# Kernel optimization log

Hardware: AMD Instinct MI355X
Metric: run time of the kernel (lower is better)

Reference implementation:

```python
import jax, jax.numpy as jnp
import numpy as np

N_ITEMS = 100000
EMBED_DIM = 64
N_REL = 3
N_EDGES = 3200000


def setup_inputs() -> dict:
    key = jax.random.key(0)
    k1, k2, k3, k4 = jax.random.split(key, 4)
    item_embeddings = jax.random.normal(k1, (N_ITEMS, EMBED_DIM), dtype=jnp.float32)
    rows = jax.random.randint(k2, (N_REL, N_EDGES), 0, N_ITEMS, dtype=jnp.int64)
    cols = jax.random.randint(k3, (N_REL, N_EDGES), 0, N_ITEMS, dtype=jnp.int64)
    vals = jax.random.uniform(k4, (N_REL, N_EDGES), dtype=jnp.float32)
    return {"item_embeddings": item_embeddings, "rows": rows, "cols": cols, "vals": vals}


def reference(item_embeddings, rows, cols, vals):
    # item_embeddings: [N, D]; rows/cols/vals: [R, E] COO edge lists per relation.
    n_items, _ = item_embeddings.shape
    n_rel = rows.shape[0]
    rel_emb = jnp.zeros_like(item_embeddings)
    for r in range(n_rel):  # fixed small number of relation types
        # SpMM: neighbor_emb[i] = sum_{e: rows[e]==i} vals[e] * E[cols[e]]
        msgs = item_embeddings[cols[r]] * vals[r][:, None]          # [E, D]
        neighbor = jax.ops.segment_sum(msgs, rows[r], num_segments=n_items)  # [N, D]
        # degree = row sum of adjacency values, clamped to min 1
        degree = jax.ops.segment_sum(vals[r], rows[r], num_segments=n_items)  # [N]
        degree = jnp.maximum(degree, 1.0)
        rel_emb = rel_emb + neighbor / degree[:, None]
    rel_emb = rel_emb / n_rel
    return item_embeddings + rel_emb
```

## Files before the change

### kernel.cpp

```cpp
#include <hip/hip_runtime.h>

#define N_ITEMS     100000
#define EMBED_DIM   64
#define N_REL       3
#define N_EDGES     3200000
#define TOTAL_EDGES (N_REL * N_EDGES)
#define NKEY        (N_REL * N_ITEMS)

#define LOG_CH   6
#define CH_ROWS  64
#define NCHUNK   1563
#define NBKT     (NCHUNK * N_REL)
#define BCAP     2368
#define LOG_CB   12
#define NCB      25
#define TILEP    2048
#define NTILEP   ((N_EDGES + TILEP - 1) / TILEP)
#define SEGSB    68
#define CBCAP    (SEGSB * TILEP)

__global__ void initall_kernel(unsigned* __restrict__ gcursorF,
                               unsigned* __restrict__ cursorC) {
    int i = blockIdx.x * 256 + threadIdx.x;
    if (i < NBKT) gcursorF[i] = (unsigned)i * (unsigned)BCAP;
    if (i < N_REL * NCB) cursorC[i] = (unsigned)(i % NCB) * (unsigned)CBCAP;
}

__global__ void tobf16_kernel(const float* __restrict__ E, unsigned short* __restrict__ Ebf) {
    int i = blockIdx.x * 256 + threadIdx.x;
    if (i < N_ITEMS * EMBED_DIM) {
        unsigned u = __float_as_uint(E[i]);
        unsigned r = (u + 0x7FFFu + ((u >> 16) & 1u)) >> 16;
        Ebf[i] = (unsigned short)r;
    }
}

__launch_bounds__(512)
__global__ void partA2_kernel(const int* __restrict__ rows,
                              const int* __restrict__ cols,
                              const float* __restrict__ vals,
                              unsigned* __restrict__ cursorC,
                              uint2* __restrict__ coarse,
                              int rel0, unsigned relStrideU2) {
    __shared__ uint2 stag[TILEP];
    __shared__ unsigned char bkt[TILEP];
    __shared__ unsigned hist[NCB], lstart[NCB], gbase[NCB], lcur[NCB];
    int rel = rel0 + blockIdx.x / NTILEP;
    int base = (blockIdx.x % NTILEP) * TILEP;
    int cnt = N_EDGES - base; if (cnt > TILEP) cnt = TILEP;
    int t = threadIdx.x;
    const int go = rel * N_EDGES + base;
    uint2* __restrict__ coarseRel = coarse + (size_t)(rel - rel0) * relStrideU2;

    unsigned rrow[4], rcol[4], rval[4];
    #pragma unroll
    for (int k = 0; k < 4; k++) {
        int i = t + (k << 9);
        if (i < cnt) {
            rrow[k] = (unsigned)rows[go + i];
            rcol[k] = (unsigned)cols[go + i];
            rval[k] = __float_as_uint(vals[go + i]);
        } else rrow[k] = 0xFFFFFFFFu;
    }
    if (t < NCB) hist[t] = 0u;
    __syncthreads();
    #pragma unroll
    for (int k = 0; k < 4; k++)
        if (rrow[k] != 0xFFFFFFFFu) atomicAdd(&hist[rrow[k] >> LOG_CB], 1u);
    __syncthreads();
    if (t < 32) {
        unsigned v = (t < NCB) ? hist[t] : 0u;
        unsigned inc = v;
        #pragma unroll
        for (int d = 1; d < 32; d <<= 1) {
            unsigned x = __shfl_up(inc, d, 32);
            if (t >= d) inc += x;
        }
        if (t < NCB) {
            unsigned ex = inc - v;
            lstart[t] = ex; lcur[t] = ex;
            if (v) gbase[t] = atomicAdd(&cursorC[rel * NCB + t], v);
        }
    }
    __syncthreads();
    #pragma unroll
    for (int k = 0; k < 4; k++)
        if (rrow[k] != 0xFFFFFFFFu) {
            unsigned row = rrow[k];
            unsigned cb = row >> LOG_CB;
            unsigned dst = atomicAdd(&lcur[cb], 1u);
            stag[dst] = make_uint2(rcol[k] | ((row & 4095u) << 17), rval[k]);
            bkt[dst] = (unsigned char)cb;
        }
    __syncthreads();
    for (int i = t; i < cnt; i += 512) {
        unsigned bb = bkt[i];
        unsigned dst = gbase[bb] + ((unsigned)i - lstart[bb]);
        if (dst < (bb + 1u) * (unsigned)CBCAP) coarseRel[dst] = stag[i];
    }
}

__launch_bounds__(512)
__global__ void partB2_kernel(const unsigned* __restrict__ cursorC,
                              const uint2* __restrict__ coarse,
                              unsigned* __restrict__ gcursorF,
                              uint2* __restrict__ recs,
                              int rel0, unsigned relStrideU2) {
    __shared__ uint2 stag[TILEP];
    __shared__ unsigned char bkt[TILEP];
    __shared__ unsigned hist[64], lstart[64], gbase[64], lcur[64];
    int rel = rel0 + blockIdx.x / (NCB * SEGSB);
    int rem = blockIdx.x % (NCB * SEGSB);
    int cb = rem / SEGSB, seg = rem % SEGSB;
    unsigned cntA = cursorC[rel * NCB + cb] - (unsigned)cb * (unsigned)CBCAP;
    if (cntA > (unsigned)CBCAP) cntA = (unsigned)CBCAP;
    int off = seg * TILEP;
    int cnt = (int)cntA - off;
    if (cnt <= 0) return;
    if (cnt > TILEP) cnt = TILEP;
    const uint2* __restrict__ src = coarse + (size_t)(rel - rel0) * relStrideU2
                                  + (unsigned)cb * (unsigned)CBCAP + off;
    int t = threadIdx.x;

    uint2 rc[4];
    #pragma unroll
    for (int k = 0; k < 4; k++) {
        int i = t + (k << 9);
        rc[k] = (i < cnt) ? src[i] : make_uint2(0xFFFFFFFFu, 0u);
    }
    if (t < 64) hist[t] = 0u;
    __syncthreads();
    #pragma unroll
    for (int k = 0; k < 4; k++)
        if (rc[k].x != 0xFFFFFFFFu) atomicAdd(&hist[(rc[k].x >> 23) & 63u], 1u);
    __syncthreads();
    if (t < 64) {
        unsigned v = hist[t];
        unsigned inc = v;
        #pragma unroll
        for (int d = 1; d < 64; d <<= 1) {
            unsigned x = __shfl_up(inc, d, 64);
            if (t >= d) inc += x;
        }
        unsigned ex = inc - v;
        lstart[t] = ex; lcur[t] = ex;
        if (v) gbase[t] = atomicAdd(&gcursorF[(((unsigned)cb << 6) + t) * 3u + rel], v);
    }
    __syncthreads();
    #pragma unroll
    for (int k = 0; k < 4; k++)
        if (rc[k].x != 0xFFFFFFFFu) {
            unsigned j = (rc[k].x >> 23) & 63u;
            unsigned dst = atomicAdd(&lcur[j], 1u);
            stag[dst] = make_uint2(rc[k].x & 0x7FFFFFu, rc[k].y);
            bkt[dst] = (unsigned char)j;
        }
    __syncthreads();
    for (int i = t; i < cnt; i += 512) {
        unsigned j = bkt[i];
        unsigned bf = (((unsigned)cb << 6) + j) * 3u + rel;
        unsigned dst = gbase[j] + ((unsigned)i - lstart[j]);
        if (dst < (bf + 1u) * (unsigned)BCAP) recs[dst] = stag[i];
    }
}

__launch_bounds__(512, 8)
__global__ void gather_sort_kernel(const uint2* __restrict__ Ebf4,
                                   const float* __restrict__ E,
                                   const unsigned* __restrict__ gcursorF,
                                   const uint2* __restrict__ recs,
                                   float* __restrict__ out) {
    __shared__ uint2  srt[BCAP];
    __shared__ float4 accT4[CH_ROWS * 16];
    __shared__ unsigned hist[CH_ROWS], cur[CH_ROWS], rstart[CH_ROWS + 1];
    int c = blockIdx.x;
    int t = threadIdx.x;
    int w = t >> 6;
    int lane = t & 63;
    int sub = lane >> 4;
    int q = lane & 15;

    float* accT = (float*)accT4;
    for (int k = t; k < CH_ROWS * EMBED_DIM; k += 512) accT[k] = 0.f;

    for (int rel = 0; rel < N_REL; rel++) {
        unsigned b = (unsigned)(c * N_REL + rel);
        unsigned s0 = b * (unsigned)BCAP;
        int n = (int)(gcursorF[b] - s0);
        if (n > BCAP) n = BCAP;
        const uint2* __restrict__ pg = recs + s0;

        uint2 rc[5];
        #pragma unroll
        for (int k = 0; k < 5; k++) {
            int i = t + (k << 9);
            rc[k] = (i < n) ? pg[i] : make_uint2(0u, 0u);
        }
        if (t < CH_ROWS) hist[t] = 0u;
        __syncthreads();
        #pragma unroll
        for (int k = 0; k < 5; k++) {
            int i = t + (k << 9);
            if (i < n) atomicAdd(&hist[rc[k].x >> 17], 1u);
        }
        __syncthreads();
        if (t < 64) {
            unsigned v = hist[t];
            unsigned inc = v;
            #pragma unroll
            for (int d = 1; d < 64; d <<= 1) {
                unsigned x = __shfl_up(inc, d, 64);
                if (lane >= d) inc += x;
            }
            rstart[t] = inc - v;
            cur[t] = inc - v;
            if (t == 63) rstart[64] = inc;
        }
        __syncthreads();
        #pragma unroll
        for (int k = 0; k < 5; k++) {
            int i = t + (k << 9);
            if (i < n) {
                unsigned pos = atomicAdd(&cur[rc[k].x >> 17], 1u);
                srt[pos] = make_uint2(rc[k].x & 0x1FFFFu, rc[k].y);
            }
        }
        __syncthreads();

        for (int k = 0; k < 8; k++) {
            int r = (w << 3) + k;
            int base = (int)rstart[r];
            int nr = (int)(rstart[r + 1] - rstart[r]);
            float a0 = 0.f, a1 = 0.f, a2 = 0.f, a3 = 0.f, dg = 0.f;
            int i = sub;
            for (; i + 12 < nr; i += 16) {
                uint2 r0 = srt[base + i],     r1 = srt[base + i + 4];
                uint2 r2 = srt[base + i + 8], r3 = srt[base + i + 12];
                uint2 e0 = Ebf4[r0.x * 16u + q];
                uint2 e1 = Ebf4[r1.x * 16u + q];
                uint2 e2 = Ebf4[r2.x * 16u + q];
                uint2 e3 = Ebf4[r3.x * 16u + q];
                float w0 = __uint_as_float(r0.y), w1 = __uint_as_float(r1.y);
                float w2 = __uint_as_float(r2.y), w3 = __uint_as_float(r3.y);
                a0 += w0 * __uint_as_float(e0.x << 16);
                a1 += w0 * __uint_as_float(e0.x & 0xFFFF0000u);
                a2 += w0 * __uint_as_float(e0.y << 16);
                a3 += w0 * __uint_as_float(e0.y & 0xFFFF0000u);
                dg += w0;
                a0 += w1 * __uint_as_float(e1.x << 16);
                a1 += w1 * __uint_as_float(e1.x & 0xFFFF0000u);
                a2 += w1 * __uint_as_float(e1.y << 16);
                a3 += w1 * __uint_as_float(e1.y & 0xFFFF0000u);
                dg += w1;
                a0 += w2 * __uint_as_float(e2.x << 16);
                a1 += w2 * __uint_as_float(e2.x & 0xFFFF0000u);
                a2 += w2 * __uint_as_float(e2.y << 16);
                a3 += w2 * __uint_as_float(e2.y & 0xFFFF0000u);
                dg += w2;
                a0 += w3 * __uint_as_float(e3.x << 16);
                a1 += w3 * __uint_as_float(e3.x & 0xFFFF0000u);
                a2 += w3 * __uint_as_float(e3.y << 16);
                a3 += w3 * __uint_as_float(e3.y & 0xFFFF0000u);
                dg += w3;
            }
            for (; i < nr; i += 4) {
                uint2 r0 = srt[base + i];
                uint2 e0 = Ebf4[r0.x * 16u + q];
                float w0 = __uint_as_float(r0.y);
                a0 += w0 * __uint_as_float(e0.x << 16);
                a1 += w0 * __uint_as_float(e0.x & 0xFFFF0000u);
                a2 += w0 * __uint_as_float(e0.y << 16);
                a3 += w0 * __uint_as_float(e0.y & 0xFFFF0000u);
                dg += w0;
            }
            a0 += __shfl_xor(a0, 16, 64);  a0 += __shfl_xor(a0, 32, 64);
            a1 += __shfl_xor(a1, 16, 64);  a1 += __shfl_xor(a1, 32, 64);
            a2 += __shfl_xor(a2, 16, 64);  a2 += __shfl_xor(a2, 32, 64);
            a3 += __shfl_xor(a3, 16, 64);  a3 += __shfl_xor(a3, 32, 64);
            dg += __shfl_xor(dg, 16, 64);  dg += __shfl_xor(dg, 32, 64);
            float inv = 1.0f / (3.0f * fmaxf(dg, 1.0f));
            if (sub == 0) {
                float4 o = accT4[(r << 4) + q];
                accT4[(r << 4) + q] = make_float4(o.x + a0 * inv, o.y + a1 * inv,
                                                  o.z + a2 * inv, o.w + a3 * inv);
            }
        }
        __syncthreads();
    }

    int gbase2 = c * (CH_ROWS * EMBED_DIM);
    for (int k = t; k < CH_ROWS * EMBED_DIM; k += 512) {
        int gi = gbase2 + k;
        if (gi < N_ITEMS * EMBED_DIM) out[gi] = E[gi] + accT[k];
    }
}

#define NBS ((NKEY + 255) / 256)

__global__ void hist300_kernel(const int* __restrict__ rows, unsigned* __restrict__ cnt) {
    int stride = gridDim.x * blockDim.x;
    for (int i = blockIdx.x * blockDim.x + threadIdx.x; i < TOTAL_EDGES; i += stride) {
        unsigned r = (unsigned)i / (unsigned)N_EDGES;
        unsigned key = r * N_ITEMS + (unsigned)rows[i];
        atomicAdd(&cnt[key], 1u);
    }
}

__global__ void scan_blocksum(const unsigned* __restrict__ cnt, unsigned* __restrict__ bsum) {
    __shared__ unsigned s[256];
    int i = blockIdx.x * 256 + threadIdx.x;
    s[threadIdx.x] = (i < NKEY) ? cnt[i] : 0u;
    __syncthreads();
    for (int off = 128; off > 0; off >>= 1) {
        if (threadIdx.x < off) s[threadIdx.x] += s[threadIdx.x + off];
        __syncthreads();
    }
    if (threadIdx.x == 0) bsum[blockIdx.x] = s[0];
}

__global__ void scan_partials(unsigned* __restrict__ bsum, unsigned* __restrict__ starts) {
    const int IT = 5;
    int t = threadIdx.x;
    unsigned loc[IT];
    unsigned sum = 0;
    #pragma unroll
    for (int k = 0; k < IT; k++) {
        int idx = t * IT + k;
        loc[k] = (idx < NBS) ? bsum[idx] : 0u;
        sum += loc[k];
    }
    int lane = t & 63, wid = t >> 6;
    unsigned inc = sum;
    #pragma unroll
    for (int d = 1; d < 64; d <<= 1) {
        unsigned x = __shfl_up(inc, d, 64);
        if (lane >= d) inc += x;
    }
    __shared__ unsigned woff[4], woffEx[4];
    if (lane == 63) woff[wid] = inc;
    __syncthreads();
    if (t == 0) { unsigned run = 0; for (int k = 0; k < 4; k++) { woffEx[k] = run; run += woff[k]; } }
    __syncthreads();
    unsigned ex = inc - sum + woffEx[wid];
    #pragma unroll
    for (int k = 0; k < IT; k++) {
        int idx = t * IT + k;
        if (idx < NBS) { bsum[idx] = ex; ex += loc[k]; }
    }
    if (t == 0) starts[NKEY] = (unsigned)TOTAL_EDGES;
}

__global__ void scan_final(unsigned* key_arr,
                           const unsigned* __restrict__ bsum,
                           unsigned* __restrict__ cursor) {
    int i = blockIdx.x * 256 + threadIdx.x;
    unsigned v = (i < NKEY) ? key_arr[i] : 0u;
    int lane = threadIdx.x & 63, wid = threadIdx.x >> 6;
    unsigned inc = v;
    #pragma unroll
    for (int d = 1; d < 64; d <<= 1) {
        unsigned x = __shfl_up(inc, d, 64);
        if (lane >= d) inc += x;
    }
    __shared__ unsigned woff[4], woffEx[4];
    if (lane == 63) woff[wid] = inc;
    __syncthreads();
    if (threadIdx.x == 0) { unsigned run = 0; for (int k = 0; k < 4; k++) { woffEx[k] = run; run += woff[k]; } }
    __syncthreads();
    unsigned ex = inc - v + woffEx[wid] + bsum[blockIdx.x];
    if (i < NKEY) { key_arr[i] = ex; cursor[i] = ex; }
}

__global__ void binscatter2_kernel(const int* __restrict__ rows,
                                   const int* __restrict__ cols,
                                   const float* __restrict__ vals,
                                   unsigned* __restrict__ cursor,
                                   uint2* __restrict__ recs) {
    int stride = gridDim.x * blockDim.x;
    for (int i = blockIdx.x * blockDim.x + threadIdx.x; i < TOTAL_EDGES; i += stride) {
        unsigned r = (unsigned)i / (unsigned)N_EDGES;
        unsigned key = r * N_ITEMS + (unsigned)rows[i];
        unsigned pos = atomicAdd(&cursor[key], 1u);
        uint2 rec;
        rec.x = (unsigned)cols[i];
        rec.y = __float_as_uint(vals[i]);
        recs[pos] = rec;
    }
}

__launch_bounds__(192)
__global__ void gather_csr_f32_kernel(const float* __restrict__ E,
                                      const unsigned* __restrict__ starts,
                                      const uint2* __restrict__ recs,
                                      float* __restrict__ out) {
    __shared__ float part[N_REL * EMBED_DIM];
    int row = blockIdx.x;
    int w = threadIdx.x >> 6;
    int d = threadIdx.x & 63;
    unsigned key = (unsigned)w * N_ITEMS + (unsigned)row;
    unsigned s = starts[key];
    int n = (int)(starts[key + 1] - s);
    const uint2* __restrict__ p = recs + s;
    float acc = 0.0f, deg = 0.0f;
    int j = 0;
    for (; j + 8 <= n; j += 8) {
        uint2 a[8];
        #pragma unroll
        for (int k = 0; k < 8; k++) a[k] = p[j + k];
        float e[8];
        #pragma unroll
        for (int k = 0; k < 8; k++) e[k] = E[a[k].x * EMBED_DIM + d];
        #pragma unroll
        for (int k = 0; k < 8; k++) {
            float wv = __uint_as_float(a[k].y);
            acc += wv * e[k];
            deg += wv;
        }
    }
    for (; j < n; j++) {
        uint2 a = p[j];
        float wv = __uint_as_float(a.y);
        acc += wv * E[a.x * EMBED_DIM + d];
        deg += wv;
    }
    part[w * EMBED_DIM + d] = acc / (3.0f * fmaxf(deg, 1.0f));
    __syncthreads();
    if (threadIdx.x < EMBED_DIM) {
        int gi = row * EMBED_DIM + threadIdx.x;
        out[gi] = E[gi] + part[threadIdx.x]
                        + part[EMBED_DIM + threadIdx.x]
                        + part[2 * EMBED_DIM + threadIdx.x];
    }
}

__global__ void deg_kernel(const int* __restrict__ rows,
                           const float* __restrict__ vals,
                           float* __restrict__ deg) {
    long long i = (long long)blockIdx.x * blockDim.x + threadIdx.x;
    if (i >= TOTAL_EDGES) return;
    int r = (int)(i / N_EDGES);
    int row = rows[i];
    atomicAdd(&deg[(long long)r * N_ITEMS + row], vals[i]);
}

__global__ void inv_kernel(float* __restrict__ deg) {
    int i = blockIdx.x * blockDim.x + threadIdx.x;
    if (i >= N_REL * N_ITEMS) return;
    float d = deg[i];
    d = fmaxf(d, 1.0f);
    deg[i] = 1.0f / (3.0f * d);
}

__global__ void scatter_kernel(const float* __restrict__ E,
                               const int* __restrict__ rows,
                               const int* __restrict__ cols,
                               const float* __restrict__ vals,
                               const float* __restrict__ inv,
                               float* __restrict__ out) {
    long long t = (long long)blockIdx.x * blockDim.x + threadIdx.x;
    long long edge = t >> 6;
    int d = (int)(t & 63);
    if (edge >= TOTAL_EDGES) return;
    int r = (int)(edge / N_EDGES);
    int row = rows[edge];
    int col = cols[edge];
    float w = vals[edge] * inv[r * N_ITEMS + row];
    float msg = w * E[(long long)col * EMBED_DIM + d];
    atomicAdd(&out[(long long)row * EMBED_DIM + d], msg);
}

extern "C" void kernel_launch(void* const* d_in, const int* in_sizes, int n_in,
                              void* d_out, int out_size, void* d_ws, size_t ws_size,
                              hipStream_t stream) {
    const float* E    = (const float*)d_in[0];
    const int*   rows = (const int*)d_in[1];
    const int*   cols = (const int*)d_in[2];
    const float* vals = (const float*)d_in[3];
    float* out = (float*)d_out;

    const size_t GCB      = 32768;
    const size_t COARSE1  = (size_t)NCB * CBCAP * sizeof(uint2);
    const size_t FINE_B   = (size_t)NBKT * BCAP * sizeof(uint2);
    const size_t EBF_B    = (size_t)N_ITEMS * EMBED_DIM * 2;
    size_t need12 = GCB + 3 * COARSE1 + FINE_B + EBF_B;
    size_t need11 = GCB + COARSE1 + FINE_B + EBF_B;

    const size_t REGA = 1204224;
    const size_t REGC = 8192;
    const size_t RECB = (size_t)TOTAL_EDGES * sizeof(uint2);
    size_t need5 = 2 * REGA + REGC + RECB;

    if (ws_size >= need12) {
        unsigned* gcursorF = (unsigned*)d_ws;
        unsigned* cursorC  = (unsigned*)((char*)d_ws + 20480);
        uint2*    coarse   = (uint2*)((char*)d_ws + GCB);
        uint2*    recs     = (uint2*)((char*)d_ws + GCB + 3 * COARSE1);
        unsigned short* Ebf = (unsigned short*)((char*)d_ws + GCB + 3 * COARSE1 + FINE_B);

        initall_kernel<<<(NBKT + 255) / 256, 256, 0, stream>>>(gcursorF, cursorC);
        tobf16_kernel<<<(N_ITEMS * EMBED_DIM + 255) / 256, 256, 0, stream>>>(E, Ebf);
        partA2_kernel<<<N_REL * NTILEP, 512, 0, stream>>>(
            rows, cols, vals, cursorC, coarse, 0, (unsigned)(NCB * CBCAP));
        partB2_kernel<<<N_REL * NCB * SEGSB, 512, 0, stream>>>(
            cursorC, coarse, gcursorF, recs, 0, (unsigned)(NCB * CBCAP));
        gather_sort_kernel<<<NCHUNK, 512, 0, stream>>>((const uint2*)Ebf, E, gcursorF, recs, out);
    } else if (ws_size >= need11) {
        unsigned* gcursorF = (unsigned*)d_ws;
        unsigned* cursorC  = (unsigned*)((char*)d_ws + 20480);
        uint2*    coarse   = (uint2*)((char*)d_ws + GCB);
        uint2*    recs     = (uint2*)((char*)d_ws + GCB + COARSE1);
        unsigned short* Ebf = (unsigned short*)((char*)d_ws + GCB + COARSE1 + FINE_B);

        initall_kernel<<<(NBKT + 255) / 256, 256, 0, stream>>>(gcursorF, cursorC);
        tobf16_kernel<<<(N_ITEMS * EMBED_DIM + 255) / 256, 256, 0, stream>>>(E, Ebf);
        for (int r = 0; r < N_REL; r++) {
            partA2_kernel<<<NTILEP, 512, 0, stream>>>(
                rows, cols, vals, cursorC, coarse, r, 0u);
            partB2_kernel<<<NCB * SEGSB, 512, 0, stream>>>(
                cursorC, coarse, gcursorF, recs, r, 0u);
        }
        gather_sort_kernel<<<NCHUNK, 512, 0, stream>>>((const uint2*)Ebf, E, gcursorF, recs, out);
    } else if (ws_size >= need5) {
        unsigned* keyA   = (unsigned*)d_ws;
        unsigned* cursor = (unsigned*)((char*)d_ws + REGA);
        unsigned* bsum   = (unsigned*)((char*)d_ws + 2 * REGA);
        uint2*    recs   = (uint2*)((char*)d_ws + 2 * REGA + REGC);

        hipMemsetAsync(keyA, 0, NKEY * sizeof(unsigned), stream);
        hist300_kernel<<<1536, 256, 0, stream>>>(rows, keyA);
        scan_blocksum<<<NBS, 256, 0, stream>>>(keyA, bsum);
        scan_partials<<<1, 256, 0, stream>>>(bsum, keyA);
        scan_final<<<NBS, 256, 0, stream>>>(keyA, bsum, cursor);
        binscatter2_kernel<<<2048, 256, 0, stream>>>(rows, cols, vals, cursor, recs);
        gather_csr_f32_kernel<<<N_ITEMS, 192, 0, stream>>>(E, keyA, recs, out);
    } else {
        float* deg = (float*)d_ws;
        hipMemsetAsync(deg, 0, (size_t)N_REL * N_ITEMS * sizeof(float), stream);
        {
            long long total = TOTAL_EDGES;
            int block = 256;
            long long grid = (total + block - 1) / block;
            deg_kernel<<<(unsigned)grid, block, 0, stream>>>(rows, vals, deg);
        }
        {
            int total = N_REL * N_ITEMS;
            int block = 256;
            int grid = (total + block - 1) / block;
            inv_kernel<<<grid, block, 0, stream>>>(deg);
        }
        hipMemcpyAsync(out, E, (size_t)N_ITEMS * EMBED_DIM * sizeof(float),
                       hipMemcpyDeviceToDevice, stream);
        {
            long long threads = (long long)TOTAL_EDGES * 64;
            int block = 256;
            long long grid = (threads + block - 1) / block;
            scatter_kernel<<<(unsigned)grid, block, 0, stream>>>(E, rows, cols, vals, deg, out);
        }
    }
}
```

Before: 396.3 us.

## Shrink partition tiles to 1024 with 256-thread blocks and fuse init kernels

Halves the partition tile size in both partitioning passes, from 2048 to 1024 edges, and uses 256-thread blocks with launch bounds allowing 8 blocks per CU. This is meant to raise occupancy and cut LDS per block. Because N_EDGES divides exactly by 1024, the tail bounds checks in partA are dropped. The cursor initialisation and the bf16 conversion are fused into one kernel that converts with float4 loads. The cost is twice as many coarse segments and blocks, so there are more global atomics on the cursors.

```diff
diff --git a/kernel.cpp b/kernel.cpp
--- a/kernel.cpp
+++ b/kernel.cpp
@@ -14,29 +14,33 @@
 #define BCAP     2368
 #define LOG_CB   12
 #define NCB      25
-#define TILEP    2048
-#define NTILEP   ((N_EDGES + TILEP - 1) / TILEP)
-#define SEGSB    68
+#define TILEP    1024
+#define NTILEP   (N_EDGES / TILEP)
+#define SEGSB    136
 #define CBCAP    (SEGSB * TILEP)
 
-__global__ void initall_kernel(unsigned* __restrict__ gcursorF,
-                               unsigned* __restrict__ cursorC) {
+__global__ void init15_kernel(const float* __restrict__ E,
+                              unsigned short* __restrict__ Ebf,
+                              unsigned* __restrict__ gcursorF,
+                              unsigned* __restrict__ cursorC) {
     int i = blockIdx.x * 256 + threadIdx.x;
     if (i < NBKT) gcursorF[i] = (unsigned)i * (unsigned)BCAP;
     if (i < N_REL * NCB) cursorC[i] = (unsigned)(i % NCB) * (unsigned)CBCAP;
-}
-
-__global__ void tobf16_kernel(const float* __restrict__ E, unsigned short* __restrict__ Ebf) {
-    int i = blockIdx.x * 256 + threadIdx.x;
-    if (i < N_ITEMS * EMBED_DIM) {
-        unsigned u = __float_as_uint(E[i]);
-        unsigned r = (u + 0x7FFFu + ((u >> 16) & 1u)) >> 16;
-        Ebf[i] = (unsigned short)r;
-    }
-}
-
-__launch_bounds__(512)
-__global__ void partA2_kernel(const int* __restrict__ rows,
+    if (i < N_ITEMS * 16) {
+        float4 f = ((const float4*)E)[i];
+        unsigned u0 = __float_as_uint(f.x), u1 = __float_as_uint(f.y);
+        unsigned u2 = __float_as_uint(f.z), u3 = __float_as_uint(f.w);
+        ushort4 o;
+        o.x = (unsigned short)((u0 + 0x7FFFu + ((u0 >> 16) & 1u)) >> 16);
+        o.y = (unsigned short)((u1 + 0x7FFFu + ((u1 >> 16) & 1u)) >> 16);
+        o.z = (unsigned short)((u2 + 0x7FFFu + ((u2 >> 16) & 1u)) >> 16);
+        o.w = (unsigned short)((u3 + 0x7FFFu + ((u3 >> 16) & 1u)) >> 16);
+        ((ushort4*)Ebf)[i] = o;
+    }
+}
+
+__launch_bounds__(256, 8)
+__global__ void partA4_kernel(const int* __restrict__ rows,
                               const int* __restrict__ cols,
                               const float* __restrict__ vals,
                               unsigned* __restrict__ cursorC,
@@ -47,7 +51,6 @@
     __shared__ unsigned hist[NCB], lstart[NCB], gbase[NCB], lcur[NCB];
     int rel = rel0 + blockIdx.x / NTILEP;
     int base = (blockIdx.x % NTILEP) * TILEP;
-    int cnt = N_EDGES - base; if (cnt > TILEP) cnt = TILEP;
     int t = threadIdx.x;
     const int go = rel * N_EDGES + base;
     uint2* __restrict__ coarseRel = coarse + (size_t)(rel - rel0) * relStrideU2;
@@ -55,18 +58,15 @@
     unsigned rrow[4], rcol[4], rval[4];
     #pragma unroll
     for (int k = 0; k < 4; k++) {
-        int i = t + (k << 9);
-        if (i < cnt) {
-            rrow[k] = (unsigned)rows[go + i];
-            rcol[k] = (unsigned)cols[go + i];
-            rval[k] = __float_as_uint(vals[go + i]);
-        } else rrow[k] = 0xFFFFFFFFu;
+        int i = t + (k << 8);
+        rrow[k] = (unsigned)rows[go + i];
+        rcol[k] = (unsigned)cols[go + i];
+        rval[k] = __float_as_uint(vals[go + i]);
     }
     if (t < NCB) hist[t] = 0u;
     __syncthreads();
     #pragma unroll
-    for (int k = 0; k < 4; k++)
-        if (rrow[k] != 0xFFFFFFFFu) atomicAdd(&hist[rrow[k] >> LOG_CB], 1u);
+    for (int k = 0; k < 4; k++) atomicAdd(&hist[rrow[k] >> LOG_CB], 1u);
     __syncthreads();
     if (t < 32) {
         unsigned v = (t < NCB) ? hist[t] : 0u;
@@ -84,24 +84,23 @@
     }
     __syncthreads();
     #pragma unroll
-    for (int k = 0; k < 4; k++)
-        if (rrow[k] != 0xFFFFFFFFu) {
-            unsigned row = rrow[k];
-            unsigned cb = row >> LOG_CB;
-            unsigned dst = atomicAdd(&lcur[cb], 1u);
-            stag[dst] = make_uint2(rcol[k] | ((row & 4095u) << 17), rval[k]);
-            bkt[dst] = (unsigned char)cb;
-        }
-    __syncthreads();
-    for (int i = t; i < cnt; i += 512) {
+    for (int k = 0; k < 4; k++) {
+        unsigned row = rrow[k];
+        unsigned cb = row >> LOG_CB;
+        unsigned dst = atomicAdd(&lcur[cb], 1u);
+        stag[dst] = make_uint2(rcol[k] | ((row & 4095u) << 17), rval[k]);
+        bkt[dst] = (unsigned char)cb;
+    }
+    __syncthreads();
+    for (int i = t; i < TILEP; i += 256) {
         unsigned bb = bkt[i];
         unsigned dst = gbase[bb] + ((unsigned)i - lstart[bb]);
         if (dst < (bb + 1u) * (unsigned)CBCAP) coarseRel[dst] = stag[i];
     }
 }
 
-__launch_bounds__(512)
-__global__ void partB2_kernel(const unsigned* __restrict__ cursorC,
+__launch_bounds__(256, 8)
+__global__ void partB4_kernel(const unsigned* __restrict__ cursorC,
                               const uint2* __restrict__ coarse,
                               unsigned* __restrict__ gcursorF,
                               uint2* __restrict__ recs,
@@ -125,7 +124,7 @@
     uint2 rc[4];
     #pragma unroll
     for (int k = 0; k < 4; k++) {
-        int i = t + (k << 9);
+        int i = t + (k << 8);
         rc[k] = (i < cnt) ? src[i] : make_uint2(0xFFFFFFFFu, 0u);
     }
     if (t < 64) hist[t] = 0u;
@@ -156,7 +155,7 @@
             bkt[dst] = (unsigned char)j;
         }
     __syncthreads();
-    for (int i = t; i < cnt; i += 512) {
+    for (int i = t; i < cnt; i += 256) {
         unsigned j = bkt[i];
         unsigned bf = (((unsigned)cb << 6) + j) * 3u + rel;
         unsigned dst = gbase[j] + ((unsigned)i - lstart[j]);
@@ -482,7 +481,7 @@
     const size_t COARSE1  = (size_t)NCB * CBCAP * sizeof(uint2);
     const size_t FINE_B   = (size_t)NBKT * BCAP * sizeof(uint2);
     const size_t EBF_B    = (size_t)N_ITEMS * EMBED_DIM * 2;
-    size_t need12 = GCB + 3 * COARSE1 + FINE_B + EBF_B;
+    size_t need15 = GCB + 3 * COARSE1 + FINE_B + EBF_B;
     size_t need11 = GCB + COARSE1 + FINE_B + EBF_B;
 
     const size_t REGA = 1204224;
@@ -490,18 +489,19 @@
     const size_t RECB = (size_t)TOTAL_EDGES * sizeof(uint2);
     size_t need5 = 2 * REGA + REGC + RECB;
 
-    if (ws_size >= need12) {
+    int initGrid = (N_ITEMS * 16 + 255) / 256;
+
+    if (ws_size >= need15) {
         unsigned* gcursorF = (unsigned*)d_ws;
         unsigned* cursorC  = (unsigned*)((char*)d_ws + 20480);
         uint2*    coarse   = (uint2*)((char*)d_ws + GCB);
         uint2*    recs     = (uint2*)((char*)d_ws + GCB + 3 * COARSE1);
         unsigned short* Ebf = (unsigned short*)((char*)d_ws + GCB + 3 * COARSE1 + FINE_B);
 
-        initall_kernel<<<(NBKT + 255) / 256, 256, 0, stream>>>(gcursorF, cursorC);
-        tobf16_kernel<<<(N_ITEMS * EMBED_DIM + 255) / 256, 256, 0, stream>>>(E, Ebf);
-        partA2_kernel<<<N_REL * NTILEP, 512, 0, stream>>>(
+        init15_kernel<<<initGrid, 256, 0, stream>>>(E, Ebf, gcursorF, cursorC);
+        partA4_kernel<<<N_REL * NTILEP, 256, 0, stream>>>(
             rows, cols, vals, cursorC, coarse, 0, (unsigned)(NCB * CBCAP));
-        partB2_kernel<<<N_REL * NCB * SEGSB, 512, 0, stream>>>(
+        partB4_kernel<<<N_REL * NCB * SEGSB, 256, 0, stream>>>(
             cursorC, coarse, gcursorF, recs, 0, (unsigned)(NCB * CBCAP));
         gather_sort_kernel<<<NCHUNK, 512, 0, stream>>>((const uint2*)Ebf, E, gcursorF, recs, out);
     } else if (ws_size >= need11) {
@@ -511,12 +511,11 @@
         uint2*    recs     = (uint2*)((char*)d_ws + GCB + COARSE1);
         unsigned short* Ebf = (unsigned short*)((char*)d_ws + GCB + COARSE1 + FINE_B);
 
-        initall_kernel<<<(NBKT + 255) / 256, 256, 0, stream>>>(gcursorF, cursorC);
-        tobf16_kernel<<<(N_ITEMS * EMBED_DIM + 255) / 256, 256, 0, stream>>>(E, Ebf);
+        init15_kernel<<<initGrid, 256, 0, stream>>>(E, Ebf, gcursorF, cursorC);
         for (int r = 0; r < N_REL; r++) {
-            partA2_kernel<<<NTILEP, 512, 0, stream>>>(
+            partA4_kernel<<<NTILEP, 256, 0, stream>>>(
                 rows, cols, vals, cursorC, coarse, r, 0u);
-            partB2_kernel<<<NCB * SEGSB, 512, 0, stream>>>(
+            partB4_kernel<<<NCB * SEGSB, 256, 0, stream>>>(
                 cursorC, coarse, gcursorF, recs, r, 0u);
         }
         gather_sort_kernel<<<NCHUNK, 512, 0, stream>>>((const uint2*)Ebf, E, gcursorF, recs, out);
```

New measurement: 441.3 us. 11.4% more time.
